# Optimization experiments

Hardware: AMD Instinct MI355X
Metric: run time of the kernel (lower is better)

Reference implementation:

```python
import jax, jax.numpy as jnp
import numpy as np

BLOCK = 128          # fp8 quantization block size (from linear_deepseek_v3)
FP8_MAX = 448.0      # max representable value of float8_e4m3fn
F8 = jnp.float8_e4m3fn
G, T, K, N = 8, 1024, 7168, 2048


def setup_inputs() -> dict:
    key = jax.random.key(0)
    kx, kw, kb = jax.random.split(key, 3)
    xs = jax.random.normal(kx, (G, T, K), jnp.float32)
    # Build an fp8 block-quantized weight + per-(128x128)-block fp32 scale,
    # matching the stored self.weight (fp8) and self.scale parameters.
    w_raw = jax.random.normal(kw, (G, N, K), jnp.float32)
    wb = w_raw.reshape(G, N // BLOCK, BLOCK, K // BLOCK, BLOCK)
    amax = jnp.max(jnp.abs(wb), axis=(2, 4))            # [G, NB, KB]
    scale = amax / FP8_MAX
    w_q = (wb / scale[:, :, None, :, None]).astype(F8).astype(jnp.float32)
    weight = w_q.reshape(G, N, K)                        # fp8 code values held in fp32
    bias = jax.random.normal(kb, (G, N), jnp.float32) * 0.02
    return {"xs": xs, "weight": weight, "scale": scale, "bias": bias}


def reference(xs, weight, scale, bias):
    """Grouped fp8 block-quantized GEMM with inline dequant.
    xs:     [G, T, K] fp32 activations (one slab per group)
    weight: [G, N, K] fp8-quantized weights (stored as fp32 code values)
    scale:  [G, N/128, K/128] fp32 per-block weight scales
    bias:   [G, N] fp32
    """
    g, t, k = xs.shape
    n = weight.shape[1]
    kb, nb = k // BLOCK, n // BLOCK
    # --- act_quant_deepseek_v3: per (token, 128-col block) absmax/448 scale ---
    xb = xs.reshape(g, t, kb, BLOCK)
    a_scale = jnp.max(jnp.abs(xb), axis=-1) / FP8_MAX        # [G, T, KB]
    x_q = (xb / a_scale[..., None]).astype(F8).astype(jnp.float32)
    x_deq = (x_q * a_scale[..., None]).reshape(g, t, k)      # fused dequant
    # --- weight dequant: broadcast per-(128x128)-block scale ---
    w_deq = (weight.reshape(g, nb, BLOCK, kb, BLOCK)
             * scale[:, :, None, :, None]).reshape(g, n, k)
    # --- grouped GEMM (y = x A^T) + bias, fp32 accumulation ---
    y = jnp.einsum('gtk,gnk->gtn', x_deq, w_deq) + bias[:, None, :]
    return y
```

## Files before the change

kernel.cpp:

```cpp
#include <hip/hip_runtime.h>
#include <hip/hip_bf16.h>
#include <stdint.h>

#define G_ 8
#define T_ 1024
#define K_ 7168
#define N_ 2048
#define KB_ 56
#define NB_ 16
#define NT8_ 56

#define ACT_WGS  57344
#define WREC_WGS 28672

typedef __attribute__((ext_vector_type(4))) float f32x4;
typedef __attribute__((ext_vector_type(8))) int   i32x8;

typedef __attribute__((address_space(3))) uint32_t lds_u32_t;
typedef const __attribute__((address_space(1))) uint32_t gbl_u32_t;

__device__ __forceinline__ void gload_lds16(const void* gsrc, const void* ldst)
{
    __builtin_amdgcn_global_load_lds(
        (gbl_u32_t*)(uintptr_t)gsrc,
        (lds_u32_t*)(uint32_t)(uintptr_t)ldst, 16, 0, 0);
}

__device__ __forceinline__ void blockbar()
{
    asm volatile("" ::: "memory");
    __builtin_amdgcn_s_barrier();
    asm volatile("" ::: "memory");
}

__global__ __launch_bounds__(256) void prep_kernel(
    const float* __restrict__ xs, uint8_t* __restrict__ xq8,
    float* __restrict__ ascale,
    const float* __restrict__ w, uint8_t* __restrict__ wq8)
{
    const int bid = blockIdx.x;
    const int tid = threadIdx.x;
    if (bid < ACT_WGS) {
        const int grp = (bid * 256 + tid) >> 5;
        const int l   = tid & 31;
        const size_t base = (size_t)grp * 128 + (size_t)l * 4;

        const float4 v = *(const float4*)(xs + base);
        float am = fmaxf(fmaxf(fabsf(v.x), fabsf(v.y)),
                         fmaxf(fabsf(v.z), fabsf(v.w)));
#pragma unroll
        for (int off = 1; off <= 16; off <<= 1)
            am = fmaxf(am, __shfl_xor(am, off, 64));

        const float rs = 448.0f / am;
        const float s  = am * (1.0f / 448.0f);

        int pk = __builtin_amdgcn_cvt_pk_fp8_f32(v.x * rs, v.y * rs, 0, false);
        pk     = __builtin_amdgcn_cvt_pk_fp8_f32(v.z * rs, v.w * rs, pk, true);
        *(uint32_t*)(xq8 + base) = (uint32_t)pk;

        if (l == 0) {
            const int kb = grp % KB_;
            const int t  = (grp / KB_) & (T_ - 1);
            const int g  = grp / (KB_ * T_);
            ascale[(((size_t)(g * 4 + (t >> 8))) * KB_ + kb) * 256 + (t & 255)] = s;
        }
    } else {
        const size_t i = ((size_t)(bid - ACT_WGS) * 256 + tid) * 16;
        uint32_t o[4];
#pragma unroll
        for (int q = 0; q < 4; ++q) {
            const float4 a = *(const float4*)(w + i + q * 4);
            int pk = __builtin_amdgcn_cvt_pk_fp8_f32(a.x, a.y, 0, false);
            pk     = __builtin_amdgcn_cvt_pk_fp8_f32(a.z, a.w, pk, true);
            o[q] = (uint32_t)pk;
        }
        *(uint4*)(wq8 + i) = make_uint4(o[0], o[1], o[2], o[3]);
    }
}

union Frag { i32x8 v; struct { int4 lo, hi; } p; };

#define RD_FRAG(dst, base, r)                                                 \
  { const int rx_ = ((r) & 7) << 4;                                           \
    const char* bp_ = smem + (base) + (r)*128;                                \
    dst.p.lo = *(const int4*)(bp_ + ((lhi*32) ^ rx_));                        \
    dst.p.hi = *(const int4*)(bp_ + ((lhi*32 + 16) ^ rx_)); }

#define STG_A(c, t, bb) gload_lds16(pA8[c] + (size_t)(t)*128,                 \
      smem + (bb)*32768 + (c)*4096 + ptid*16)
#define STG_B(c, t, bb) gload_lds16(pB8[c] + (size_t)(t)*128,                 \
      smem + 98304 + (bb)*16384 + (c)*4096 + ptid*16)
#define STG_S(c) gload_lds16(pS + (size_t)(c)*1024,                           \
      smem + 147456 + ((c)&1)*4096 + ptid*16)

__global__ __launch_bounds__(768, 1) void gemm_fp8_kernel(
    const uint8_t* __restrict__ xq8, const uint8_t* __restrict__ wq8,
    const float* __restrict__ ascale, const float* __restrict__ wscale,
    const float* __restrict__ bias, float* __restrict__ y)
{
    __shared__ char smem[155904];

    const int bx0 = blockIdx.x;
    const int g     = bx0 & 7;
    const int inner = bx0 >> 3;
    const int tm    = inner & 3;
    const int tn    = inner >> 2;
    const int t0 = tm * 256, n0 = tn * 128;

    const int tid  = threadIdx.x, lane = tid & 63, wid = tid >> 6;
    const bool producer = (wid >= 8);
    const int ptid = tid & 255;
    const int l15 = lane & 15, lhi = lane >> 4;
    const int wrow = (wid >> 1) * 64;
    const int wcol = (wid & 1) * 64;

    const uint8_t* Ag = xq8 + (size_t)g * T_ * K_;
    const uint8_t* Bg = wq8 + (size_t)g * N_ * K_;

    const int srow = ptid >> 3;
    const int xoff = ((ptid & 7) ^ (srow & 7)) * 16;
    const uint8_t* pA8[8];
    const uint8_t* pB8[4];
#pragma unroll
    for (int c = 0; c < 8; ++c)
        pA8[c] = Ag + (size_t)(t0 + c * 32 + srow) * K_ + xoff;
#pragma unroll
    for (int c = 0; c < 4; ++c)
        pB8[c] = Bg + (size_t)(n0 + c * 32 + srow) * K_ + xoff;

    const float* pS = ascale + ((size_t)(g * 4 + tm) * KB_) * 256 + ptid * 4;

    const f32x4 z4 = {0.f, 0.f, 0.f, 0.f};
    f32x4 acc[4][4] = {};
    Frag bF[4];
    f32x4 asv[4];

    if (producer) {
        if (ptid < KB_) {
            const float wv = wscale[((size_t)(g * NB_ + tn)) * KB_ + ptid];
            *(float*)(smem + 155648 + ptid * 4) = wv;
        }
        STG_S(0);
#pragma unroll
        for (int c = 0; c < 8; ++c) STG_A(c, 0, 0);
#pragma unroll
        for (int c = 0; c < 4; ++c) STG_B(c, 0, 0);
#pragma unroll
        for (int c = 0; c < 8; ++c) STG_A(c, 1, 1);
#pragma unroll
        for (int c = 0; c < 4; ++c) STG_B(c, 1, 1);
        asm volatile("s_waitcnt vmcnt(12)" ::: "memory");
        asm volatile("s_waitcnt lgkmcnt(0)" ::: "memory");
    } else {
        __builtin_amdgcn_s_setprio(1);
    }
    blockbar();

    int cur = 0;
    for (int u = 0; u < NT8_; ++u) {
        if (producer) {
            if ((u & 3) == 0 && u + 4 < NT8_) STG_S((u >> 2) + 1);
            if (u + 2 < NT8_) {
                const int fb = (cur + 2 >= 3) ? cur - 1 : cur + 2;
#pragma unroll
                for (int c = 0; c < 8; ++c) STG_A(c, u + 2, fb);
#pragma unroll
                for (int c = 0; c < 4; ++c) STG_B(c, u + 2, fb);
                asm volatile("s_waitcnt vmcnt(12)" ::: "memory");
            } else if (u + 1 < NT8_) {
                asm volatile("s_waitcnt vmcnt(0)" ::: "memory");
            }
        } else {
            const float wsc = *(const float*)(smem + 155648 + u * 4);
            const int abase = cur * 32768;
            const int bbase = 98304 + cur * 16384;
            const int sbuf = (u >> 2) & 1;

#pragma unroll
            for (int n = 0; n < 4; ++n)
                RD_FRAG(bF[n], bbase, wcol + n * 16 + l15);
#pragma unroll
            for (int m = 0; m < 4; ++m) {
                const float4 sv = *(const float4*)(smem + 147456 + sbuf * 4096 +
                    (u & 3) * 1024 + (wrow + m * 16 + lhi * 4) * 4);
                asv[m][0] = sv.x * wsc; asv[m][1] = sv.y * wsc;
                asv[m][2] = sv.z * wsc; asv[m][3] = sv.w * wsc;
            }

#pragma unroll
            for (int m = 0; m < 4; ++m) {
                Frag aF;
                RD_FRAG(aF, abase, wrow + m * 16 + l15);
#pragma unroll
                for (int n = 0; n < 4; ++n) {
                    f32x4 blk = __builtin_amdgcn_mfma_scale_f32_16x16x128_f8f6f4(
                        aF.v, bF[n].v, z4, 0, 0, 0, 0x7F7F7F7F, 0, 0x7F7F7F7F);
                    acc[m][n] += blk * asv[m];
                }
            }
        }

        blockbar();
        cur = (cur + 1 >= 3) ? 0 : cur + 1;
    }

    if (!producer) {
        float* Yg = y + (size_t)g * T_ * N_;
#pragma unroll
        for (int n = 0; n < 4; ++n) {
            const int col = n0 + wcol + n * 16 + l15;
            const float bv = bias[g * N_ + col];
#pragma unroll
            for (int m = 0; m < 4; ++m) {
                const int r0 = t0 + wrow + m * 16 + lhi * 4;
#pragma unroll
                for (int j = 0; j < 4; ++j)
                    Yg[(size_t)(r0 + j) * N_ + col] = acc[m][n][j] + bv;
            }
        }
    }
}

extern "C" void kernel_launch(void* const* d_in, const int* in_sizes, int n_in,
                              void* d_out, int out_size, void* d_ws, size_t ws_size,
                              hipStream_t stream)
{
    const float* xs     = (const float*)d_in[0];
    const float* weight = (const float*)d_in[1];
    const float* scale  = (const float*)d_in[2];
    const float* bias   = (const float*)d_in[3];
    float* y = (float*)d_out;

    uint8_t* xq8  = (uint8_t*)d_ws;
    float*   ascl = (float*)((char*)d_ws + 58720256);
    uint8_t* wq8  = (uint8_t*)((char*)d_ws + 60555264);

    prep_kernel<<<ACT_WGS + WREC_WGS, 256, 0, stream>>>(
        xs, xq8, ascl, weight, wq8);

    gemm_fp8_kernel<<<G_ * (T_ / 256) * (N_ / 128), 768, 0, stream>>>(
        xq8, wq8, ascl, scale, bias, y);
}
```

Before: 318.9 us.

## Fuse weight fp8 conversion into GEMM producer instead of separate prep pass

New measurement: 835.3 us. 2.62x slower.

```diff
diff --git a/kernel.cpp b/kernel.cpp
--- a/kernel.cpp
+++ b/kernel.cpp
@@ -11,7 +11,6 @@
 #define NT8_ 56
 
 #define ACT_WGS  57344
-#define WREC_WGS 28672
 
 typedef __attribute__((ext_vector_type(4))) float f32x4;
 typedef __attribute__((ext_vector_type(8))) int   i32x8;
@@ -35,47 +34,33 @@
 
 __global__ __launch_bounds__(256) void prep_kernel(
     const float* __restrict__ xs, uint8_t* __restrict__ xq8,
-    float* __restrict__ ascale,
-    const float* __restrict__ w, uint8_t* __restrict__ wq8)
+    float* __restrict__ ascale)
 {
     const int bid = blockIdx.x;
     const int tid = threadIdx.x;
-    if (bid < ACT_WGS) {
-        const int grp = (bid * 256 + tid) >> 5;
-        const int l   = tid & 31;
-        const size_t base = (size_t)grp * 128 + (size_t)l * 4;
-
-        const float4 v = *(const float4*)(xs + base);
-        float am = fmaxf(fmaxf(fabsf(v.x), fabsf(v.y)),
-                         fmaxf(fabsf(v.z), fabsf(v.w)));
-#pragma unroll
-        for (int off = 1; off <= 16; off <<= 1)
-            am = fmaxf(am, __shfl_xor(am, off, 64));
-
-        const float rs = 448.0f / am;
-        const float s  = am * (1.0f / 448.0f);
-
-        int pk = __builtin_amdgcn_cvt_pk_fp8_f32(v.x * rs, v.y * rs, 0, false);
-        pk     = __builtin_amdgcn_cvt_pk_fp8_f32(v.z * rs, v.w * rs, pk, true);
-        *(uint32_t*)(xq8 + base) = (uint32_t)pk;
-
-        if (l == 0) {
-            const int kb = grp % KB_;
-            const int t  = (grp / KB_) & (T_ - 1);
-            const int g  = grp / (KB_ * T_);
-            ascale[(((size_t)(g * 4 + (t >> 8))) * KB_ + kb) * 256 + (t & 255)] = s;
-        }
-    } else {
-        const size_t i = ((size_t)(bid - ACT_WGS) * 256 + tid) * 16;
-        uint32_t o[4];
-#pragma unroll
-        for (int q = 0; q < 4; ++q) {
-            const float4 a = *(const float4*)(w + i + q * 4);
-            int pk = __builtin_amdgcn_cvt_pk_fp8_f32(a.x, a.y, 0, false);
-            pk     = __builtin_amdgcn_cvt_pk_fp8_f32(a.z, a.w, pk, true);
-            o[q] = (uint32_t)pk;
-        }
-        *(uint4*)(wq8 + i) = make_uint4(o[0], o[1], o[2], o[3]);
+    const int grp = (bid * 256 + tid) >> 5;
+    const int l   = tid & 31;
+    const size_t base = (size_t)grp * 128 + (size_t)l * 4;
+
+    const float4 v = *(const float4*)(xs + base);
+    float am = fmaxf(fmaxf(fabsf(v.x), fabsf(v.y)),
+                     fmaxf(fabsf(v.z), fabsf(v.w)));
+#pragma unroll
+    for (int off = 1; off <= 16; off <<= 1)
+        am = fmaxf(am, __shfl_xor(am, off, 64));
+
+    const float rs = 448.0f / am;
+    const float s  = am * (1.0f / 448.0f);
+
+    int pk = __builtin_amdgcn_cvt_pk_fp8_f32(v.x * rs, v.y * rs, 0, false);
+    pk     = __builtin_amdgcn_cvt_pk_fp8_f32(v.z * rs, v.w * rs, pk, true);
+    *(uint32_t*)(xq8 + base) = (uint32_t)pk;
+
+    if (l == 0) {
+        const int kb = grp % KB_;
+        const int t  = (grp / KB_) & (T_ - 1);
+        const int g  = grp / (KB_ * T_);
+        ascale[(((size_t)(g * 4 + (t >> 8))) * KB_ + kb) * 256 + (t & 255)] = s;
     }
 }
 
@@ -89,13 +74,25 @@
 
 #define STG_A(c, t, bb) gload_lds16(pA8[c] + (size_t)(t)*128,                 \
       smem + (bb)*32768 + (c)*4096 + ptid*16)
-#define STG_B(c, t, bb) gload_lds16(pB8[c] + (size_t)(t)*128,                 \
-      smem + 98304 + (bb)*16384 + (c)*4096 + ptid*16)
 #define STG_S(c) gload_lds16(pS + (size_t)(c)*1024,                           \
       smem + 147456 + ((c)&1)*4096 + ptid*16)
 
+#define LOAD_B16(t)                                                           \
+  { _Pragma("unroll") for (int q = 0; q < 16; ++q)                            \
+      br[q] = *(const f32x4*)(pWf + (size_t)q * 8 * K_ + (size_t)(t) * 128); }
+
+#define CVT_WRITE_B(bb)                                                       \
+  { _Pragma("unroll") for (int q = 0; q < 16; ++q) {                          \
+      int pk_ = __builtin_amdgcn_cvt_pk_fp8_f32(br[q][0], br[q][1], 0, false);\
+      pk_ = __builtin_amdgcn_cvt_pk_fp8_f32(br[q][2], br[q][3], pk_, true);   \
+      const int r_ = q * 8 + (ptid >> 5);                                     \
+      *(uint32_t*)(smem + 98304 + (bb)*16384 + r_*128 +                       \
+          ((((ptid & 31) >> 2) ^ (r_ & 7)) << 4) + (ptid & 3) * 4) =          \
+          (uint32_t)pk_;                                                      \
+  } }
+
 __global__ __launch_bounds__(768, 1) void gemm_fp8_kernel(
-    const uint8_t* __restrict__ xq8, const uint8_t* __restrict__ wq8,
+    const uint8_t* __restrict__ xq8, const float* __restrict__ w,
     const float* __restrict__ ascale, const float* __restrict__ wscale,
     const float* __restrict__ bias, float* __restrict__ y)
 {
@@ -116,18 +113,16 @@
     const int wcol = (wid & 1) * 64;
 
     const uint8_t* Ag = xq8 + (size_t)g * T_ * K_;
-    const uint8_t* Bg = wq8 + (size_t)g * N_ * K_;
+    const float*   Wg = w   + (size_t)g * N_ * K_;
 
     const int srow = ptid >> 3;
     const int xoff = ((ptid & 7) ^ (srow & 7)) * 16;
     const uint8_t* pA8[8];
-    const uint8_t* pB8[4];
 #pragma unroll
     for (int c = 0; c < 8; ++c)
         pA8[c] = Ag + (size_t)(t0 + c * 32 + srow) * K_ + xoff;
-#pragma unroll
-    for (int c = 0; c < 4; ++c)
-        pB8[c] = Bg + (size_t)(n0 + c * 32 + srow) * K_ + xoff;
+
+    const float* pWf = Wg + (size_t)(n0 + (ptid >> 5)) * K_ + (ptid & 31) * 4;
 
     const float* pS = ascale + ((size_t)(g * 4 + tm) * KB_) * 256 + ptid * 4;
 
@@ -135,6 +130,7 @@
     f32x4 acc[4][4] = {};
     Frag bF[4];
     f32x4 asv[4];
+    f32x4 br[16];
 
     if (producer) {
         if (ptid < KB_) {
@@ -144,13 +140,12 @@
         STG_S(0);
 #pragma unroll
         for (int c = 0; c < 8; ++c) STG_A(c, 0, 0);
-#pragma unroll
-        for (int c = 0; c < 4; ++c) STG_B(c, 0, 0);
+        LOAD_B16(0);
+        asm volatile("s_waitcnt vmcnt(0)" ::: "memory");
+        CVT_WRITE_B(0);
 #pragma unroll
         for (int c = 0; c < 8; ++c) STG_A(c, 1, 1);
-#pragma unroll
-        for (int c = 0; c < 4; ++c) STG_B(c, 1, 1);
-        asm volatile("s_waitcnt vmcnt(12)" ::: "memory");
+        LOAD_B16(1);
         asm volatile("s_waitcnt lgkmcnt(0)" ::: "memory");
     } else {
         __builtin_amdgcn_s_setprio(1);
@@ -160,16 +155,21 @@
     int cur = 0;
     for (int u = 0; u < NT8_; ++u) {
         if (producer) {
-            if ((u & 3) == 0 && u + 4 < NT8_) STG_S((u >> 2) + 1);
             if (u + 2 < NT8_) {
                 const int fb = (cur + 2 >= 3) ? cur - 1 : cur + 2;
+                const int nb = (cur + 1 >= 3) ? 0 : cur + 1;
 #pragma unroll
                 for (int c = 0; c < 8; ++c) STG_A(c, u + 2, fb);
-#pragma unroll
-                for (int c = 0; c < 4; ++c) STG_B(c, u + 2, fb);
-                asm volatile("s_waitcnt vmcnt(12)" ::: "memory");
+                asm volatile("s_waitcnt vmcnt(8)" ::: "memory");
+                CVT_WRITE_B(nb);
+                LOAD_B16(u + 2);
+                if ((u & 3) == 0 && u + 4 < NT8_) STG_S((u >> 2) + 1);
+                asm volatile("s_waitcnt lgkmcnt(0)" ::: "memory");
             } else if (u + 1 < NT8_) {
+                const int nb = (cur + 1 >= 3) ? 0 : cur + 1;
                 asm volatile("s_waitcnt vmcnt(0)" ::: "memory");
+                CVT_WRITE_B(nb);
+                asm volatile("s_waitcnt lgkmcnt(0)" ::: "memory");
             }
         } else {
             const float wsc = *(const float*)(smem + 155648 + u * 4);
@@ -234,11 +234,9 @@
 
     uint8_t* xq8  = (uint8_t*)d_ws;
     float*   ascl = (float*)((char*)d_ws + 58720256);
-    uint8_t* wq8  = (uint8_t*)((char*)d_ws + 60555264);
-
-    prep_kernel<<<ACT_WGS + WREC_WGS, 256, 0, stream>>>(
-        xs, xq8, ascl, weight, wq8);
+
+    prep_kernel<<<ACT_WGS, 256, 0, stream>>>(xs, xq8, ascl);
 
     gemm_fp8_kernel<<<G_ * (T_ / 256) * (N_ / 128), 768, 0, stream>>>(
-        xq8, wq8, ascl, scale, bias, y);
-}
+        xq8, weight, ascl, scale, bias, y);
+}
```

## Double-buffer B fragments in registers and unroll consumer loop by two

Applied to the files above, without the earlier changes.

Measured after the change: 508.8 us. 1.6x slower.

```diff
diff --git a/kernel.cpp b/kernel.cpp
--- a/kernel.cpp
+++ b/kernel.cpp
@@ -94,6 +94,42 @@
 #define STG_S(c) gload_lds16(pS + (size_t)(c)*1024,                           \
       smem + 147456 + ((c)&1)*4096 + ptid*16)
 
+#define PROD_BODY(u_)                                                         \
+  { if (((u_) & 3) == 0 && (u_) + 4 < NT8_) STG_S(((u_) >> 2) + 1);           \
+    if ((u_) + 2 < NT8_) {                                                    \
+      const int fb_ = ((u_) + 2) % 3;                                         \
+      _Pragma("unroll") for (int c = 0; c < 8; ++c) STG_A(c, (u_) + 2, fb_);  \
+      _Pragma("unroll") for (int c = 0; c < 4; ++c) STG_B(c, (u_) + 2, fb_);  \
+    }                                                                         \
+    asm volatile("s_waitcnt vmcnt(0)" ::: "memory"); }
+
+#define CONS_BODY(u_, CUR, NXT, PF_)                                          \
+  { const int cb_ = (u_) % 3;                                                 \
+    const float wsc_ = *(const float*)(smem + 155648 + (u_) * 4);             \
+    if (PF_) {                                                                \
+      const int nb_ = ((u_) + 1) % 3;                                         \
+      _Pragma("unroll") for (int n = 0; n < 4; ++n)                           \
+        RD_FRAG(bF##NXT[n], 98304 + nb_ * 16384, wcol + n * 16 + l15);        \
+    }                                                                         \
+    const int sb_ = ((u_) >> 2) & 1;                                          \
+    __builtin_amdgcn_s_setprio(1);                                            \
+    _Pragma("unroll") for (int m = 0; m < 4; ++m) {                           \
+      Frag aF;                                                                \
+      RD_FRAG(aF, cb_ * 32768, wrow + m * 16 + l15);                          \
+      const float4 sv = *(const float4*)(smem + 147456 + sb_ * 4096 +         \
+          ((u_) & 3) * 1024 + (wrow + m * 16 + lhi * 4) * 4);                 \
+      f32x4 asv_;                                                             \
+      asv_[0] = sv.x * wsc_; asv_[1] = sv.y * wsc_;                           \
+      asv_[2] = sv.z * wsc_; asv_[3] = sv.w * wsc_;                           \
+      _Pragma("unroll") for (int n = 0; n < 4; ++n) {                         \
+        f32x4 blk = __builtin_amdgcn_mfma_scale_f32_16x16x128_f8f6f4(         \
+            aF.v, bF##CUR[n].v, z4, 0, 0, 0, 0x7F7F7F7F, 0, 0x7F7F7F7F);      \
+        acc[m][n] += blk * asv_;                                              \
+      }                                                                       \
+    }                                                                         \
+    __builtin_amdgcn_s_setprio(0);                                            \
+  }
+
 __global__ __launch_bounds__(768, 1) void gemm_fp8_kernel(
     const uint8_t* __restrict__ xq8, const uint8_t* __restrict__ wq8,
     const float* __restrict__ ascale, const float* __restrict__ wscale,
@@ -133,8 +169,7 @@
 
     const f32x4 z4 = {0.f, 0.f, 0.f, 0.f};
     f32x4 acc[4][4] = {};
-    Frag bF[4];
-    f32x4 asv[4];
+    Frag bFA[4], bFB[4];
 
     if (producer) {
         if (ptid < KB_) {
@@ -150,59 +185,25 @@
         for (int c = 0; c < 8; ++c) STG_A(c, 1, 1);
 #pragma unroll
         for (int c = 0; c < 4; ++c) STG_B(c, 1, 1);
-        asm volatile("s_waitcnt vmcnt(12)" ::: "memory");
+        asm volatile("s_waitcnt vmcnt(0)" ::: "memory");
         asm volatile("s_waitcnt lgkmcnt(0)" ::: "memory");
-    } else {
-        __builtin_amdgcn_s_setprio(1);
     }
     blockbar();
 
-    int cur = 0;
-    for (int u = 0; u < NT8_; ++u) {
-        if (producer) {
-            if ((u & 3) == 0 && u + 4 < NT8_) STG_S((u >> 2) + 1);
-            if (u + 2 < NT8_) {
-                const int fb = (cur + 2 >= 3) ? cur - 1 : cur + 2;
-#pragma unroll
-                for (int c = 0; c < 8; ++c) STG_A(c, u + 2, fb);
-#pragma unroll
-                for (int c = 0; c < 4; ++c) STG_B(c, u + 2, fb);
-                asm volatile("s_waitcnt vmcnt(12)" ::: "memory");
-            } else if (u + 1 < NT8_) {
-                asm volatile("s_waitcnt vmcnt(0)" ::: "memory");
-            }
-        } else {
-            const float wsc = *(const float*)(smem + 155648 + u * 4);
-            const int abase = cur * 32768;
-            const int bbase = 98304 + cur * 16384;
-            const int sbuf = (u >> 2) & 1;
-
-#pragma unroll
-            for (int n = 0; n < 4; ++n)
-                RD_FRAG(bF[n], bbase, wcol + n * 16 + l15);
-#pragma unroll
-            for (int m = 0; m < 4; ++m) {
-                const float4 sv = *(const float4*)(smem + 147456 + sbuf * 4096 +
-                    (u & 3) * 1024 + (wrow + m * 16 + lhi * 4) * 4);
-                asv[m][0] = sv.x * wsc; asv[m][1] = sv.y * wsc;
-                asv[m][2] = sv.z * wsc; asv[m][3] = sv.w * wsc;
-            }
-
-#pragma unroll
-            for (int m = 0; m < 4; ++m) {
-                Frag aF;
-                RD_FRAG(aF, abase, wrow + m * 16 + l15);
-#pragma unroll
-                for (int n = 0; n < 4; ++n) {
-                    f32x4 blk = __builtin_amdgcn_mfma_scale_f32_16x16x128_f8f6f4(
-                        aF.v, bF[n].v, z4, 0, 0, 0, 0x7F7F7F7F, 0, 0x7F7F7F7F);
-                    acc[m][n] += blk * asv[m];
-                }
-            }
-        }
-
+    if (!producer) {
+#pragma unroll
+        for (int n = 0; n < 4; ++n)
+            RD_FRAG(bFA[n], 98304, wcol + n * 16 + l15);
+    }
+
+    for (int v = 0; v < NT8_ / 2; ++v) {
+        const int u0 = 2 * v, u1 = 2 * v + 1;
+        if (producer) { PROD_BODY(u0); }
+        else          { CONS_BODY(u0, A, B, true); }
         blockbar();
-        cur = (cur + 1 >= 3) ? 0 : cur + 1;
+        if (producer) { PROD_BODY(u1); }
+        else          { CONS_BODY(u1, B, A, (u1 + 1 < NT8_)); }
+        blockbar();
     }
 
     if (!producer) {
```
